# Kernel optimization log

Measured on AMD Instinct MI355X. Metric: run time of the kernel, lower is better.

## Reference

```python
import jax, jax.numpy as jnp
import numpy as np

T, N, H, D = 128, 2048, 128, 128  # timesteps, envs, hidden_dim, embedding_dim
EPS = 1e-5


def layer_norm(x, w, b):
    m = x.mean(-1, keepdims=True)
    v = ((x - m) ** 2).mean(-1, keepdims=True)
    return (x - m) * jax.lax.rsqrt(v + EPS) * w + b


def setup_inputs() -> dict:
    key = jax.random.key(0)
    ks = jax.random.split(key, 10)
    s = 0.05
    return {
        "x": jax.random.normal(ks[0], (T * N, D), jnp.float32),
        "hxs": jax.random.normal(ks[1], (N, 1, H), jnp.float32),
        "masks": jax.random.randint(ks[2], (T * N, 1), 0, 2).astype(jnp.float32),
        "ln1_w": jnp.ones((D,), jnp.float32),
        "ln1_b": jnp.zeros((D,), jnp.float32),
        "W1": jax.random.normal(ks[3], (H, D), jnp.float32) * s,
        "b1": jnp.zeros((H,), jnp.float32),
        "W2": jax.random.normal(ks[4], (H, H), jnp.float32) * s,
        "b2": jnp.zeros((H,), jnp.float32),
        "W_ih": jax.random.normal(ks[5], (3 * H, H), jnp.float32) * s,
        "b_ih": jnp.zeros((3 * H,), jnp.float32),
        "W_hh": jax.random.normal(ks[6], (3 * H, H), jnp.float32) * s,
        "b_hh": jnp.zeros((3 * H,), jnp.float32),
        "ln2_w": jnp.ones((H,), jnp.float32),
        "ln2_b": jnp.zeros((H,), jnp.float32),
    }


def reference(x, hxs, masks, ln1_w, ln1_b, W1, b1, W2, b2,
              W_ih, b_ih, W_hh, b_hh, ln2_w, ln2_b):
    # feature norm + two linear layers (no nonlinearity in the original)
    feats = layer_norm(x, ln1_w, ln1_b)            # [T*N, D]
    feats = feats @ W1.T + b1                      # [T*N, H]
    feats = feats @ W2.T + b2                      # [T*N, H]
    feats = feats.reshape(T, N, H)
    m = masks.reshape(T, N)

    # precompute input-side GRU gates once (big GEMM outside the scan)
    gi = feats @ W_ih.T + b_ih                     # [T, N, 3H]

    h0 = hxs[:, 0, :]                              # num_rnn_layers == 1

    def step(h, inp):
        gi_t, m_t = inp
        h = h * m_t[:, None]                       # mask-reset (== segment split)
        gh = h @ W_hh.T + b_hh                     # [N, 3H]
        i_r, i_z, i_n = jnp.split(gi_t, 3, axis=-1)
        h_r, h_z, h_n = jnp.split(gh, 3, axis=-1)
        r = jax.nn.sigmoid(i_r + h_r)
        z = jax.nn.sigmoid(i_z + h_z)
        n = jnp.tanh(i_n + r * h_n)
        h_new = (1.0 - z) * n + z * h
        return h_new, h_new

    hT, outs = jax.lax.scan(step, h0, (gi, m))     # outs: [T, N, H]

    out = layer_norm(outs.reshape(T * N, H), ln2_w, ln2_b)
    return out, hT[:, None, :]
```

## Files before the change

kernel.cpp:

```cpp
#include <hip/hip_runtime.h>
#include <hip/hip_bf16.h>

#define Tt 128
#define Nn 2048
#define Hh 128
#define Dd 128
#define NB 8
#define LDA 136
#define LDG 388

typedef __attribute__((ext_vector_type(8))) short v8s;
typedef __attribute__((ext_vector_type(4))) float v4f;

__device__ __forceinline__ unsigned short f2bf(float f) {
    unsigned int u = __builtin_bit_cast(unsigned int, f);
    u += 0x7FFFu + ((u >> 16) & 1u);
    return (unsigned short)(u >> 16);
}

__device__ __forceinline__ v4f mfma_bf(v8s a, v8s b, v4f c) {
    return __builtin_amdgcn_mfma_f32_16x16x32_bf16(a, b, c, 0, 0, 0);
}

__device__ __forceinline__ v8s load_wfrag_bf(const float* __restrict__ W, int row, int k0) {
    const v4f* p = (const v4f*)(W + row * 128 + k0);
    v4f a = p[0], b = p[1];
    v8s r;
    r[0] = (short)f2bf(a[0]); r[1] = (short)f2bf(a[1]);
    r[2] = (short)f2bf(a[2]); r[3] = (short)f2bf(a[3]);
    r[4] = (short)f2bf(b[0]); r[5] = (short)f2bf(b[1]);
    r[6] = (short)f2bf(b[2]); r[7] = (short)f2bf(b[3]);
    return r;
}

__device__ __forceinline__ void store_bf4(unsigned short* p, v4f v) {
    unsigned int lo = ((unsigned int)f2bf(v[1]) << 16) | (unsigned int)f2bf(v[0]);
    unsigned int hi = ((unsigned int)f2bf(v[3]) << 16) | (unsigned int)f2bf(v[2]);
    uint2 d; d.x = lo; d.y = hi;
    *(uint2*)p = d;
}

__device__ __forceinline__ float sigm(float x) { return __frcp_rn(1.f + __expf(-x)); }
__device__ __forceinline__ float tanh_f(float x) {
    return 2.f * __frcp_rn(1.f + __expf(-2.f * x)) - 1.f;
}

__global__ __launch_bounds__(512, 2)
void rppo_pipe(const float* __restrict__ x, const float* __restrict__ hxs,
               const float* __restrict__ masks,
               const float* __restrict__ ln1_w, const float* __restrict__ ln1_b,
               const float* __restrict__ W1, const float* __restrict__ b1,
               const float* __restrict__ W2, const float* __restrict__ b2,
               const float* __restrict__ Wih, const float* __restrict__ bih,
               const float* __restrict__ Whh, const float* __restrict__ bhh,
               const float* __restrict__ ln2_w, const float* __restrict__ ln2_b,
               float* __restrict__ out)
{
    __shared__ unsigned short fbuf[16 * LDA];
    __shared__ unsigned short abuf[16 * LDA];
    __shared__ unsigned short bbuf[16 * LDA];
    __shared__ unsigned short hbuf[16 * LDA];
    __shared__ float gibuf[8 * LDG];
    __shared__ float ghbuf[8 * LDG];
    __shared__ float mbuf[Tt * NB];

    const int tid  = threadIdx.x;
    const int wave = tid >> 6;
    const int lane = tid & 63;
    const int l16  = lane & 15;
    const int quad = lane >> 4;
    const int arow = l16 & 7;
    const int wsub = wave & 3;
    const bool isP = (wave < 4);
    const int n0   = blockIdx.x * NB;

    v8s wreg[10][4];
    float brA[2], brB[2], brC[6];
    if (isP) {
#pragma unroll
        for (int c = 0; c < 2; ++c) {
            int rowc = (2 * wsub + c) * 16 + l16;
            brA[c] = b1[rowc];
            brB[c] = b2[rowc];
#pragma unroll
            for (int kk = 0; kk < 4; ++kk) {
                int k0 = kk * 32 + quad * 8;
                wreg[c][kk]     = load_wfrag_bf(W1, rowc, k0);
                wreg[2 + c][kk] = load_wfrag_bf(W2, rowc, k0);
            }
        }
#pragma unroll
        for (int c = 0; c < 6; ++c) {
            int rowc = (6 * wsub + c) * 16 + l16;
            brC[c] = bih[rowc];
#pragma unroll
            for (int kk = 0; kk < 4; ++kk)
                wreg[4 + c][kk] = load_wfrag_bf(Wih, rowc, kk * 32 + quad * 8);
        }
    } else {
#pragma unroll
        for (int c = 0; c < 6; ++c) {
            int rowc = (6 * wsub + c) * 16 + l16;
            brC[c] = bhh[rowc];
#pragma unroll
            for (int kk = 0; kk < 4; ++kk)
                wreg[4 + c][kk] = load_wfrag_bf(Whh, rowc, kk * 32 + quad * 8);
        }
    }

    for (int i = tid; i < Tt * NB; i += 512) {
        int t = i >> 3, b = i & 7;
        mbuf[i] = masks[t * Nn + n0 + b];
    }

    const int col4 = (tid & 31) << 2;
    const int row8 = tid >> 5;
    const int prow = (wave - 4) * 2 + (lane >> 5);

    v4f ln1w, ln1b, ln2w, ln2b, h, xv;
    if (isP) {
        ln1w = *(const v4f*)(ln1_w + col4);
        ln1b = *(const v4f*)(ln1_b + col4);
        xv = *(const v4f*)(x + (size_t)(n0 + row8) * Dd + col4);
    } else {
        ln2w = *(const v4f*)(ln2_w + col4);
        ln2b = *(const v4f*)(ln2_b + col4);
        h = *(const v4f*)(hxs + (size_t)(n0 + prow) * Hh + col4);
        h *= masks[n0 + prow];
        store_bf4(hbuf + prow * LDA + col4, h);
    }
    __syncthreads();

    for (int i = 0; i <= Tt; ++i) {
        if (isP) {
            if (i < Tt) {
                float s  = xv[0] + xv[1] + xv[2] + xv[3];
                float ss = xv[0]*xv[0] + xv[1]*xv[1] + xv[2]*xv[2] + xv[3]*xv[3];
#pragma unroll
                for (int m = 1; m < 32; m <<= 1) {
                    s  += __shfl_xor(s,  m, 64);
                    ss += __shfl_xor(ss, m, 64);
                }
                float mu = s * (1.f / 128.f);
                float rs = __frsqrt_rn(ss * (1.f / 128.f) - mu * mu + 1e-5f);
                v4f f;
#pragma unroll
                for (int e = 0; e < 4; ++e) f[e] = (xv[e] - mu) * rs * ln1w[e] + ln1b[e];
                store_bf4(fbuf + row8 * LDA + col4, f);
                if (i + 1 < Tt)
                    xv = *(const v4f*)(x + ((size_t)(i + 1) * Nn + n0 + row8) * Dd + col4);
            }
        } else if (i >= 1) {
            const int t = i - 1;
            const float* gb = gibuf + prow * LDG + col4;
            const float* hb = ghbuf + prow * LDG + col4;
            v4f ir  = *(const v4f*)(gb);
            v4f iz  = *(const v4f*)(gb + 128);
            v4f inn = *(const v4f*)(gb + 256);
            v4f hr  = *(const v4f*)(hb);
            v4f hz  = *(const v4f*)(hb + 128);
            v4f hn  = *(const v4f*)(hb + 256);
            v4f hnew;
#pragma unroll
            for (int e = 0; e < 4; ++e) {
                float r = sigm(ir[e] + hr[e]);
                float z = sigm(iz[e] + hz[e]);
                float n = tanh_f(inn[e] + r * hn[e]);
                hnew[e] = n + z * (h[e] - n);
            }
            float s2  = hnew[0] + hnew[1] + hnew[2] + hnew[3];
            float ss2 = hnew[0]*hnew[0] + hnew[1]*hnew[1] + hnew[2]*hnew[2] + hnew[3]*hnew[3];
#pragma unroll
            for (int m = 1; m < 32; m <<= 1) {
                s2  += __shfl_xor(s2,  m, 64);
                ss2 += __shfl_xor(ss2, m, 64);
            }
            float mu2 = s2 * (1.f / 128.f);
            float rs2 = __frsqrt_rn(ss2 * (1.f / 128.f) - mu2 * mu2 + 1e-5f);
            v4f o;
#pragma unroll
            for (int e = 0; e < 4; ++e) o[e] = (hnew[e] - mu2) * rs2 * ln2w[e] + ln2b[e];
            *(v4f*)(out + ((size_t)t * Nn + n0 + prow) * Hh + col4) = o;

            if (t + 1 < Tt) {
                float mt = mbuf[(t + 1) * NB + prow];
                h = hnew * mt;
                store_bf4(hbuf + prow * LDA + col4, h);
            } else {
                *(v4f*)(out + (size_t)Tt * Nn * Hh + (size_t)(n0 + prow) * Hh + col4) = hnew;
            }
        }
        __syncthreads();

        if (isP && i < Tt) {
            v8s af[4];
#pragma unroll
            for (int kk = 0; kk < 4; ++kk)
                af[kk] = *(const v8s*)(fbuf + arow * LDA + kk * 32 + quad * 8);
            v4f acc[2] = {{0.f,0.f,0.f,0.f},{0.f,0.f,0.f,0.f}};
#pragma unroll
            for (int c = 0; c < 2; ++c)
#pragma unroll
                for (int kk = 0; kk < 4; ++kk)
                    acc[c] = mfma_bf(af[kk], wreg[c][kk], acc[c]);
#pragma unroll
            for (int c = 0; c < 2; ++c) {
                int col = (2 * wsub + c) * 16 + l16;
#pragma unroll
                for (int rr = 0; rr < 4; ++rr) {
                    int row = quad * 4 + rr;
                    if (row < 8) abuf[row * LDA + col] = f2bf(acc[c][rr] + brA[c]);
                }
            }
        }
        __syncthreads();

        if (isP && i < Tt) {
            v8s af[4];
#pragma unroll
            for (int kk = 0; kk < 4; ++kk)
                af[kk] = *(const v8s*)(abuf + arow * LDA + kk * 32 + quad * 8);
            v4f acc[2] = {{0.f,0.f,0.f,0.f},{0.f,0.f,0.f,0.f}};
#pragma unroll
            for (int c = 0; c < 2; ++c)
#pragma unroll
                for (int kk = 0; kk < 4; ++kk)
                    acc[c] = mfma_bf(af[kk], wreg[2 + c][kk], acc[c]);
#pragma unroll
            for (int c = 0; c < 2; ++c) {
                int col = (2 * wsub + c) * 16 + l16;
#pragma unroll
                for (int rr = 0; rr < 4; ++rr) {
                    int row = quad * 4 + rr;
                    if (row < 8) bbuf[row * LDA + col] = f2bf(acc[c][rr] + brB[c]);
                }
            }
        }
        __syncthreads();

        if (i < Tt) {
            const unsigned short* srcA = isP ? bbuf : hbuf;
            float* dst = isP ? gibuf : ghbuf;
            v8s af[4];
#pragma unroll
            for (int kk = 0; kk < 4; ++kk)
                af[kk] = *(const v8s*)(srcA + arow * LDA + kk * 32 + quad * 8);
            v4f acc[6];
#pragma unroll
            for (int c = 0; c < 6; ++c) acc[c] = (v4f){0.f,0.f,0.f,0.f};
#pragma unroll
            for (int c = 0; c < 6; ++c)
#pragma unroll
                for (int kk = 0; kk < 4; ++kk)
                    acc[c] = mfma_bf(af[kk], wreg[4 + c][kk], acc[c]);
#pragma unroll
            for (int c = 0; c < 6; ++c) {
                int col = (6 * wsub + c) * 16 + l16;
#pragma unroll
                for (int rr = 0; rr < 4; ++rr) {
                    int row = quad * 4 + rr;
                    if (row < 8) dst[row * LDG + col] = acc[c][rr] + brC[c];
                }
            }
        }
        __syncthreads();
    }
}

extern "C" void kernel_launch(void* const* d_in, const int* in_sizes, int n_in,
                              void* d_out, int out_size, void* d_ws, size_t ws_size,
                              hipStream_t stream) {
    const float* x     = (const float*)d_in[0];
    const float* hxs   = (const float*)d_in[1];
    const float* masks = (const float*)d_in[2];
    const float* ln1w  = (const float*)d_in[3];
    const float* ln1b  = (const float*)d_in[4];
    const float* W1    = (const float*)d_in[5];
    const float* b1    = (const float*)d_in[6];
    const float* W2    = (const float*)d_in[7];
    const float* b2    = (const float*)d_in[8];
    const float* Wih   = (const float*)d_in[9];
    const float* bih   = (const float*)d_in[10];
    const float* Whh   = (const float*)d_in[11];
    const float* bhh   = (const float*)d_in[12];
    const float* ln2w  = (const float*)d_in[13];
    const float* ln2b  = (const float*)d_in[14];
    float* out = (float*)d_out;

    hipLaunchKernelGGL(rppo_pipe, dim3(Nn / NB), dim3(512), 0, stream,
                       x, hxs, masks, ln1w, ln1b, W1, b1, W2, b2,
                       Wih, bih, Whh, bhh, ln2w, ln2b, out);
}
```

Measured before the change: 577.3 us.

## Fold W1, W2, Wih into one combined weight and collapse per-step GEMM chain

Since the two linear layers and the GRU input projection have no nonlinearity between them, two small prep kernels precompute Wc = Wih·W2·W1 and the matching combined bias into workspace. The scan kernel then does a single 128→384 MFMA per step for the input side instead of three chained GEMMs, which removes two barriers per timestep. It also rebalances the elementwise work across all 8 waves (one row per wave, two columns per lane) and replaces __syncthreads with a raw waitcnt+s_barrier. The trade-off is two extra launches and a different bf16 rounding path, since the product is formed in fp32 and rounded once instead of after each layer.

```diff
diff --git a/kernel.cpp b/kernel.cpp
--- a/kernel.cpp
+++ b/kernel.cpp
@@ -1,5 +1,4 @@
 #include <hip/hip_runtime.h>
-#include <hip/hip_bf16.h>
 
 #define Tt 128
 #define Nn 2048
@@ -9,8 +8,14 @@
 #define LDA 136
 #define LDG 388
 
+#define WC_OFF  0
+#define BC_OFF  49152
+#define TMP_OFF 49536
+#define BT_OFF  65920
+
 typedef __attribute__((ext_vector_type(8))) short v8s;
 typedef __attribute__((ext_vector_type(4))) float v4f;
+typedef __attribute__((ext_vector_type(2))) float v2f;
 
 __device__ __forceinline__ unsigned short f2bf(float f) {
     unsigned int u = __builtin_bit_cast(unsigned int, f);
@@ -33,35 +38,58 @@
     return r;
 }
 
-__device__ __forceinline__ void store_bf4(unsigned short* p, v4f v) {
-    unsigned int lo = ((unsigned int)f2bf(v[1]) << 16) | (unsigned int)f2bf(v[0]);
-    unsigned int hi = ((unsigned int)f2bf(v[3]) << 16) | (unsigned int)f2bf(v[2]);
-    uint2 d; d.x = lo; d.y = hi;
-    *(uint2*)p = d;
-}
-
 __device__ __forceinline__ float sigm(float x) { return __frcp_rn(1.f + __expf(-x)); }
 __device__ __forceinline__ float tanh_f(float x) {
     return 2.f * __frcp_rn(1.f + __expf(-2.f * x)) - 1.f;
 }
 
+#define BARRIER() asm volatile("s_waitcnt lgkmcnt(0)\n\ts_barrier" ::: "memory")
+
+__global__ void prep_tmp(const float* __restrict__ W1, const float* __restrict__ b1,
+                         const float* __restrict__ W2, const float* __restrict__ b2,
+                         float* __restrict__ ws) {
+    float* Tmp = ws + TMP_OFF;
+    float* bt  = ws + BT_OFF;
+    int j = blockIdx.x, d = threadIdx.x;
+    float acc = 0.f;
+    for (int k = 0; k < 128; ++k) acc += W2[j * 128 + k] * W1[k * 128 + d];
+    Tmp[j * 128 + d] = acc;
+    if (d == 0) {
+        float s = 0.f;
+        for (int k = 0; k < 128; ++k) s += W2[j * 128 + k] * b1[k];
+        bt[j] = s + b2[j];
+    }
+}
+
+__global__ void prep_wc(const float* __restrict__ Wih, const float* __restrict__ bih,
+                        float* __restrict__ ws) {
+    const float* Tmp = ws + TMP_OFF;
+    const float* bt  = ws + BT_OFF;
+    float* Wc = ws + WC_OFF;
+    float* bc = ws + BC_OFF;
+    int r = blockIdx.x, d = threadIdx.x;
+    float acc = 0.f;
+    for (int j = 0; j < 128; ++j) acc += Wih[r * 128 + j] * Tmp[j * 128 + d];
+    Wc[r * 128 + d] = acc;
+    if (d == 0) {
+        float s = 0.f;
+        for (int j = 0; j < 128; ++j) s += Wih[r * 128 + j] * bt[j];
+        bc[r] = s + bih[r];
+    }
+}
+
 __global__ __launch_bounds__(512, 2)
-void rppo_pipe(const float* __restrict__ x, const float* __restrict__ hxs,
+void rppo_scan(const float* __restrict__ x, const float* __restrict__ hxs,
                const float* __restrict__ masks,
                const float* __restrict__ ln1_w, const float* __restrict__ ln1_b,
-               const float* __restrict__ W1, const float* __restrict__ b1,
-               const float* __restrict__ W2, const float* __restrict__ b2,
-               const float* __restrict__ Wih, const float* __restrict__ bih,
                const float* __restrict__ Whh, const float* __restrict__ bhh,
                const float* __restrict__ ln2_w, const float* __restrict__ ln2_b,
-               float* __restrict__ out)
+               const float* __restrict__ ws, float* __restrict__ out)
 {
-    __shared__ unsigned short fbuf[16 * LDA];
-    __shared__ unsigned short abuf[16 * LDA];
-    __shared__ unsigned short bbuf[16 * LDA];
-    __shared__ unsigned short hbuf[16 * LDA];
-    __shared__ float gibuf[8 * LDG];
-    __shared__ float ghbuf[8 * LDG];
+    __shared__ unsigned short fbuf[NB * LDA];
+    __shared__ unsigned short hbuf[NB * LDA];
+    __shared__ float gibuf[NB * LDG];
+    __shared__ float ghbuf[NB * LDG];
     __shared__ float mbuf[Tt * NB];
 
     const int tid  = threadIdx.x;
@@ -73,186 +101,127 @@
     const int wsub = wave & 3;
     const bool isP = (wave < 4);
     const int n0   = blockIdx.x * NB;
-
-    v8s wreg[10][4];
-    float brA[2], brB[2], brC[6];
-    if (isP) {
-#pragma unroll
-        for (int c = 0; c < 2; ++c) {
-            int rowc = (2 * wsub + c) * 16 + l16;
-            brA[c] = b1[rowc];
-            brB[c] = b2[rowc];
-#pragma unroll
-            for (int kk = 0; kk < 4; ++kk) {
-                int k0 = kk * 32 + quad * 8;
-                wreg[c][kk]     = load_wfrag_bf(W1, rowc, k0);
-                wreg[2 + c][kk] = load_wfrag_bf(W2, rowc, k0);
-            }
-        }
+    const int r    = wave;
+    const int c2   = lane << 1;
+
+    const float* Wc = ws + WC_OFF;
+    const float* bc = ws + BC_OFF;
+
+    v8s wreg[6][4];
+    float brC[6];
+    {
+        const float* Wm = isP ? Wc : Whh;
+        const float* bm = isP ? bc : bhh;
 #pragma unroll
         for (int c = 0; c < 6; ++c) {
             int rowc = (6 * wsub + c) * 16 + l16;
-            brC[c] = bih[rowc];
+            brC[c] = bm[rowc];
 #pragma unroll
             for (int kk = 0; kk < 4; ++kk)
-                wreg[4 + c][kk] = load_wfrag_bf(Wih, rowc, kk * 32 + quad * 8);
-        }
-    } else {
-#pragma unroll
-        for (int c = 0; c < 6; ++c) {
-            int rowc = (6 * wsub + c) * 16 + l16;
-            brC[c] = bhh[rowc];
-#pragma unroll
-            for (int kk = 0; kk < 4; ++kk)
-                wreg[4 + c][kk] = load_wfrag_bf(Whh, rowc, kk * 32 + quad * 8);
-        }
-    }
-
-    for (int i = tid; i < Tt * NB; i += 512) {
-        int t = i >> 3, b = i & 7;
-        mbuf[i] = masks[t * Nn + n0 + b];
-    }
-
-    const int col4 = (tid & 31) << 2;
-    const int row8 = tid >> 5;
-    const int prow = (wave - 4) * 2 + (lane >> 5);
-
-    v4f ln1w, ln1b, ln2w, ln2b, h, xv;
-    if (isP) {
-        ln1w = *(const v4f*)(ln1_w + col4);
-        ln1b = *(const v4f*)(ln1_b + col4);
-        xv = *(const v4f*)(x + (size_t)(n0 + row8) * Dd + col4);
-    } else {
-        ln2w = *(const v4f*)(ln2_w + col4);
-        ln2b = *(const v4f*)(ln2_b + col4);
-        h = *(const v4f*)(hxs + (size_t)(n0 + prow) * Hh + col4);
-        h *= masks[n0 + prow];
-        store_bf4(hbuf + prow * LDA + col4, h);
-    }
+                wreg[c][kk] = load_wfrag_bf(Wm, rowc, kk * 32 + quad * 8);
+        }
+    }
+
+    for (int idx = tid; idx < Tt * NB; idx += 512) {
+        int t = idx >> 3, b = idx & 7;
+        mbuf[idx] = masks[t * Nn + n0 + b];
+    }
+
+    v2f ln1w2 = *(const v2f*)(ln1_w + c2);
+    v2f ln1b2 = *(const v2f*)(ln1_b + c2);
+    v2f ln2w2 = *(const v2f*)(ln2_w + c2);
+    v2f ln2b2 = *(const v2f*)(ln2_b + c2);
+
+    v2f h = *(const v2f*)(hxs + (size_t)(n0 + r) * Hh + c2);
+    float m0 = masks[n0 + r];
+    h[0] *= m0; h[1] *= m0;
+    *(unsigned int*)(hbuf + r * LDA + c2) =
+        (unsigned int)f2bf(h[0]) | ((unsigned int)f2bf(h[1]) << 16);
+
+    v2f xv = *(const v2f*)(x + (size_t)(n0 + r) * Dd + c2);
+
     __syncthreads();
 
     for (int i = 0; i <= Tt; ++i) {
-        if (isP) {
-            if (i < Tt) {
-                float s  = xv[0] + xv[1] + xv[2] + xv[3];
-                float ss = xv[0]*xv[0] + xv[1]*xv[1] + xv[2]*xv[2] + xv[3]*xv[3];
-#pragma unroll
-                for (int m = 1; m < 32; m <<= 1) {
-                    s  += __shfl_xor(s,  m, 64);
-                    ss += __shfl_xor(ss, m, 64);
-                }
-                float mu = s * (1.f / 128.f);
-                float rs = __frsqrt_rn(ss * (1.f / 128.f) - mu * mu + 1e-5f);
-                v4f f;
-#pragma unroll
-                for (int e = 0; e < 4; ++e) f[e] = (xv[e] - mu) * rs * ln1w[e] + ln1b[e];
-                store_bf4(fbuf + row8 * LDA + col4, f);
-                if (i + 1 < Tt)
-                    xv = *(const v4f*)(x + ((size_t)(i + 1) * Nn + n0 + row8) * Dd + col4);
-            }
-        } else if (i >= 1) {
+        if (i >= 1) {
             const int t = i - 1;
-            const float* gb = gibuf + prow * LDG + col4;
-            const float* hb = ghbuf + prow * LDG + col4;
-            v4f ir  = *(const v4f*)(gb);
-            v4f iz  = *(const v4f*)(gb + 128);
-            v4f inn = *(const v4f*)(gb + 256);
-            v4f hr  = *(const v4f*)(hb);
-            v4f hz  = *(const v4f*)(hb + 128);
-            v4f hn  = *(const v4f*)(hb + 256);
-            v4f hnew;
-#pragma unroll
-            for (int e = 0; e < 4; ++e) {
-                float r = sigm(ir[e] + hr[e]);
-                float z = sigm(iz[e] + hz[e]);
-                float n = tanh_f(inn[e] + r * hn[e]);
-                hnew[e] = n + z * (h[e] - n);
-            }
-            float s2  = hnew[0] + hnew[1] + hnew[2] + hnew[3];
-            float ss2 = hnew[0]*hnew[0] + hnew[1]*hnew[1] + hnew[2]*hnew[2] + hnew[3]*hnew[3];
-#pragma unroll
-            for (int m = 1; m < 32; m <<= 1) {
+            const float* gb = gibuf + r * LDG + c2;
+            const float* hb = ghbuf + r * LDG + c2;
+            v2f ir  = *(const v2f*)(gb);
+            v2f iz  = *(const v2f*)(gb + 128);
+            v2f inn = *(const v2f*)(gb + 256);
+            v2f hr  = *(const v2f*)(hb);
+            v2f hz  = *(const v2f*)(hb + 128);
+            v2f hn  = *(const v2f*)(hb + 256);
+            float hn0, hn1;
+            {
+                float rg = sigm(ir[0] + hr[0]);
+                float z  = sigm(iz[0] + hz[0]);
+                float n  = tanh_f(inn[0] + rg * hn[0]);
+                hn0 = n + z * (h[0] - n);
+            }
+            {
+                float rg = sigm(ir[1] + hr[1]);
+                float z  = sigm(iz[1] + hz[1]);
+                float n  = tanh_f(inn[1] + rg * hn[1]);
+                hn1 = n + z * (h[1] - n);
+            }
+            float s2 = hn0 + hn1, ss2 = hn0 * hn0 + hn1 * hn1;
+#pragma unroll
+            for (int m = 1; m < 64; m <<= 1) {
                 s2  += __shfl_xor(s2,  m, 64);
                 ss2 += __shfl_xor(ss2, m, 64);
             }
             float mu2 = s2 * (1.f / 128.f);
             float rs2 = __frsqrt_rn(ss2 * (1.f / 128.f) - mu2 * mu2 + 1e-5f);
-            v4f o;
-#pragma unroll
-            for (int e = 0; e < 4; ++e) o[e] = (hnew[e] - mu2) * rs2 * ln2w[e] + ln2b[e];
-            *(v4f*)(out + ((size_t)t * Nn + n0 + prow) * Hh + col4) = o;
+            v2f o;
+            o[0] = (hn0 - mu2) * rs2 * ln2w2[0] + ln2b2[0];
+            o[1] = (hn1 - mu2) * rs2 * ln2w2[1] + ln2b2[1];
+            *(v2f*)(out + ((size_t)t * Nn + n0 + r) * Hh + c2) = o;
 
             if (t + 1 < Tt) {
-                float mt = mbuf[(t + 1) * NB + prow];
-                h = hnew * mt;
-                store_bf4(hbuf + prow * LDA + col4, h);
+                float mt = mbuf[(t + 1) * NB + r];
+                h[0] = hn0 * mt; h[1] = hn1 * mt;
+                *(unsigned int*)(hbuf + r * LDA + c2) =
+                    (unsigned int)f2bf(h[0]) | ((unsigned int)f2bf(h[1]) << 16);
             } else {
-                *(v4f*)(out + (size_t)Tt * Nn * Hh + (size_t)(n0 + prow) * Hh + col4) = hnew;
-            }
-        }
-        __syncthreads();
-
-        if (isP && i < Tt) {
+                v2f hf; hf[0] = hn0; hf[1] = hn1;
+                *(v2f*)(out + (size_t)Tt * Nn * Hh + (size_t)(n0 + r) * Hh + c2) = hf;
+            }
+        }
+        if (i < Tt) {
+            float s = xv[0] + xv[1], ss = xv[0] * xv[0] + xv[1] * xv[1];
+#pragma unroll
+            for (int m = 1; m < 64; m <<= 1) {
+                s  += __shfl_xor(s,  m, 64);
+                ss += __shfl_xor(ss, m, 64);
+            }
+            float mu = s * (1.f / 128.f);
+            float rs = __frsqrt_rn(ss * (1.f / 128.f) - mu * mu + 1e-5f);
+            float f0 = (xv[0] - mu) * rs * ln1w2[0] + ln1b2[0];
+            float f1 = (xv[1] - mu) * rs * ln1w2[1] + ln1b2[1];
+            *(unsigned int*)(fbuf + r * LDA + c2) =
+                (unsigned int)f2bf(f0) | ((unsigned int)f2bf(f1) << 16);
+            if (i + 1 < Tt)
+                xv = *(const v2f*)(x + ((size_t)(i + 1) * Nn + n0 + r) * Dd + c2);
+        }
+        BARRIER();
+
+        if (i < Tt) {
+            const unsigned short* src = isP ? fbuf : hbuf;
+            float* dst = isP ? gibuf : ghbuf;
             v8s af[4];
 #pragma unroll
             for (int kk = 0; kk < 4; ++kk)
-                af[kk] = *(const v8s*)(fbuf + arow * LDA + kk * 32 + quad * 8);
-            v4f acc[2] = {{0.f,0.f,0.f,0.f},{0.f,0.f,0.f,0.f}};
-#pragma unroll
-            for (int c = 0; c < 2; ++c)
+                af[kk] = *(const v8s*)(src + arow * LDA + kk * 32 + quad * 8);
+            v4f acc[6];
+#pragma unroll
+            for (int c = 0; c < 6; ++c) acc[c] = (v4f){0.f, 0.f, 0.f, 0.f};
+#pragma unroll
+            for (int c = 0; c < 6; ++c)
 #pragma unroll
                 for (int kk = 0; kk < 4; ++kk)
                     acc[c] = mfma_bf(af[kk], wreg[c][kk], acc[c]);
-#pragma unroll
-            for (int c = 0; c < 2; ++c) {
-                int col = (2 * wsub + c) * 16 + l16;
-#pragma unroll
-                for (int rr = 0; rr < 4; ++rr) {
-                    int row = quad * 4 + rr;
-                    if (row < 8) abuf[row * LDA + col] = f2bf(acc[c][rr] + brA[c]);
-                }
-            }
-        }
-        __syncthreads();
-
-        if (isP && i < Tt) {
-            v8s af[4];
-#pragma unroll
-            for (int kk = 0; kk < 4; ++kk)
-                af[kk] = *(const v8s*)(abuf + arow * LDA + kk * 32 + quad * 8);
-            v4f acc[2] = {{0.f,0.f,0.f,0.f},{0.f,0.f,0.f,0.f}};
-#pragma unroll
-            for (int c = 0; c < 2; ++c)
-#pragma unroll
-                for (int kk = 0; kk < 4; ++kk)
-                    acc[c] = mfma_bf(af[kk], wreg[2 + c][kk], acc[c]);
-#pragma unroll
-            for (int c = 0; c < 2; ++c) {
-                int col = (2 * wsub + c) * 16 + l16;
-#pragma unroll
-                for (int rr = 0; rr < 4; ++rr) {
-                    int row = quad * 4 + rr;
-                    if (row < 8) bbuf[row * LDA + col] = f2bf(acc[c][rr] + brB[c]);
-                }
-            }
-        }
-        __syncthreads();
-
-        if (i < Tt) {
-            const unsigned short* srcA = isP ? bbuf : hbuf;
-            float* dst = isP ? gibuf : ghbuf;
-            v8s af[4];
-#pragma unroll
-            for (int kk = 0; kk < 4; ++kk)
-                af[kk] = *(const v8s*)(srcA + arow * LDA + kk * 32 + quad * 8);
-            v4f acc[6];
-#pragma unroll
-            for (int c = 0; c < 6; ++c) acc[c] = (v4f){0.f,0.f,0.f,0.f};
-#pragma unroll
-            for (int c = 0; c < 6; ++c)
-#pragma unroll
-                for (int kk = 0; kk < 4; ++kk)
-                    acc[c] = mfma_bf(af[kk], wreg[4 + c][kk], acc[c]);
 #pragma unroll
             for (int c = 0; c < 6; ++c) {
                 int col = (6 * wsub + c) * 16 + l16;
@@ -263,7 +232,7 @@
                 }
             }
         }
-        __syncthreads();
+        BARRIER();
     }
 }
 
@@ -286,8 +255,12 @@
     const float* ln2w  = (const float*)d_in[13];
     const float* ln2b  = (const float*)d_in[14];
     float* out = (float*)d_out;
-
-    hipLaunchKernelGGL(rppo_pipe, dim3(Nn / NB), dim3(512), 0, stream,
-                       x, hxs, masks, ln1w, ln1b, W1, b1, W2, b2,
-                       Wih, bih, Whh, bhh, ln2w, ln2b, out);
-}
+    float* ws  = (float*)d_ws;
+
+    hipLaunchKernelGGL(prep_tmp, dim3(128), dim3(128), 0, stream, W1, b1, W2, b2, ws);
+    hipLaunchKernelGGL(prep_wc,  dim3(384), dim3(128), 0, stream, Wih, bih, ws);
+
+    hipLaunchKernelGGL(rppo_scan, dim3(Nn / NB), dim3(512), 0, stream,
+                       x, hxs, masks, ln1w, ln1b, Whh, bhh, ln2w, ln2b,
+                       (const float*)ws, out);
+}
```

Measured after the change: 470.7 us. -18.5%, faster.
